# Performance work log

Hardware: AMD Instinct MI355X
Metric: run time of the kernel (lower is better)

## Reference

```python
import jax, jax.numpy as jnp
import numpy as np

IN_F = 2048
OUT_F = 2048
NNZ = 1048576
B = 8192


def setup_inputs() -> dict:
    key = jax.random.key(0)
    k1, k2, k3 = jax.random.split(key, 3)
    x = jax.random.normal(k1, (B, IN_F), dtype=jnp.float32)
    weights = (jax.random.normal(k2, (NNZ,), dtype=jnp.float32) * 0.02).astype(jnp.float16)
    coords = jax.random.randint(k3, (NNZ,), 0, OUT_F * IN_F, dtype=jnp.int64)
    return {"x": x, "weights": weights, "coords": coords}


def reference(x, weights, coords):
    # COO SpMV: out[b, row] += w * x[b, col] for each (row, col, w) triple.
    # coords are flat indices into the [OUT_F, IN_F] weight matrix.
    rows = coords // IN_F
    cols = coords % IN_F
    # Scatter-accumulate sparse weights into a dense matrix (duplicates add,
    # matching the kernel's atomic accumulation), then one batched matmul
    # replaces the per-row kernel launches of the original.
    W = jnp.zeros((OUT_F, IN_F), dtype=jnp.float32)
    W = W.at[rows, cols].add(weights.astype(jnp.float32))
    out = jnp.einsum('bi,oi->bo', x, W)  # [B, OUT_F] fp32, like the CL buffer
    return out.astype(x.dtype)
```

## Files before the change

kernel.cpp:

```cpp
#include <hip/hip_runtime.h>
#include <hip/hip_fp16.h>

#define IN_F   2048
#define OUT_F  2048
#define NNZ_   1048576
#define BATCH  8192
#define W_ROW0 6144
#define W_BASE ((size_t)W_ROW0 * OUT_F)

typedef __bf16 bf16x8 __attribute__((ext_vector_type(8)));
typedef float  f32x4  __attribute__((ext_vector_type(4)));

__device__ __forceinline__ float bfval(unsigned short b) {
    union { unsigned int u; float f; } t; t.u = ((unsigned int)b) << 16; return t.f;
}
__device__ __forceinline__ unsigned short f2bf(float f) {
    union { float f; unsigned int u; } v; v.f = f;
    unsigned int u = v.u; u += 0x7FFF + ((u >> 16) & 1);
    return (unsigned short)(u >> 16);
}
__device__ __forceinline__ float h2f(unsigned short b) {
    union { unsigned short u; __half h; } t; t.u = b; return __half2float(t.h);
}
__device__ __forceinline__ void gload_lds16(const void* g, void* l) {
    __builtin_amdgcn_global_load_lds(
        (const __attribute__((address_space(1))) unsigned int*)g,
        (__attribute__((address_space(3))) unsigned int*)l,
        16, 0, 0);
}

__global__ void prep_kernel(const float4* __restrict__ x,
                            ushort4* __restrict__ xb,
                            float4* __restrict__ Wz) {
    const int stride = gridDim.x * blockDim.x;
    const int t0 = blockIdx.x * blockDim.x + threadIdx.x;
    for (int i = t0; i < OUT_F * IN_F / 4; i += stride)
        Wz[i] = float4{0.f, 0.f, 0.f, 0.f};
    for (int i = t0; i < BATCH * IN_F / 4; i += stride) {
        float4 v = x[i];
        ushort4 o;
        o.x = f2bf(v.x); o.y = f2bf(v.y); o.z = f2bf(v.z); o.w = f2bf(v.w);
        xb[i] = o;
    }
}

__global__ void scatter_w_kernel(const unsigned short* __restrict__ wbits,
                                 const int* __restrict__ coords,
                                 float* __restrict__ W, int nnz) {
    __shared__ unsigned int sbf, sfh;
    if (threadIdx.x == 0) { sbf = 0u; sfh = 0u; }
    __syncthreads();
    unsigned int mbf = 0u, mfh = 0u;
    for (int i = threadIdx.x; i < 512; i += blockDim.x) {
        unsigned short b = wbits[i];
        unsigned int abf = (((unsigned int)b) << 16) & 0x7FFFFFFFu;
        unsigned int afh = (unsigned int)(b & 0x7FFF);
        mbf = mbf > abf ? mbf : abf;
        mfh = mfh > afh ? mfh : afh;
    }
    atomicMax(&sbf, mbf); atomicMax(&sfh, mfh);
    __syncthreads();
    union { unsigned int u; float f; } tb; tb.u = sbf;
    float bmax = tb.f;
    float hmax = h2f((unsigned short)sfh);
    int mode = (bmax > 1e-3f && bmax < 16.f) ? 0
             : (hmax > 1e-3f && hmax < 16.f) ? 1 : 2;

    int i = blockIdx.x * blockDim.x + threadIdx.x;
    if (i < nnz) {
        float v;
        if (mode == 0)      v = bfval(wbits[i]);
        else if (mode == 1) v = h2f(wbits[i]);
        else                v = ((const float*)wbits)[i];
        atomicAdd(&W[coords[i] & (OUT_F * IN_F - 1)], v);
    }
}

__global__ void f32_to_bf16_kernel(const float4* __restrict__ in,
                                   ushort4* __restrict__ out, int n4) {
    int s = gridDim.x * blockDim.x;
    for (int i = blockIdx.x * blockDim.x + threadIdx.x; i < n4; i += s) {
        float4 v = in[i];
        ushort4 o;
        o.x = f2bf(v.x); o.y = f2bf(v.y); o.z = f2bf(v.z); o.w = f2bf(v.w);
        out[i] = o;
    }
}

__global__ __launch_bounds__(512, 1) void gemm256_kernel(
    const unsigned short* __restrict__ xb,
    const unsigned short* __restrict__ wb,
    float* __restrict__ out) {
    constexpr int K = IN_F;
    constexpr int NT = K / 64;

    __shared__ __align__(16) unsigned short As[2][256 * 64];
    __shared__ __align__(16) unsigned short Bs[2][256 * 64];

    const int tid  = threadIdx.x;
    const int lane = tid & 63;
    const int wave = tid >> 6;
    const int wr   = wave >> 2;
    const int wc   = wave & 3;
    const int frow = lane & 15;
    const int klan = lane >> 4;
    const int s0   = klan ^ (lane & 7);

    const int flat = blockIdx.x;
    const int swz  = (flat & 7) * 32 + (flat >> 3);
    const int tm   = swz & 31;
    const int tn   = swz >> 5;

    const unsigned short* srcA = xb + (size_t)tm * 256 * K;
    const unsigned short* srcB = wb + (size_t)tn * 256 * K;

    const int rloc  = lane >> 3;
    const int sslot = (lane & 7) ^ rloc;

    f32x4 acc[8][4] = {};

    auto stage = [&](int buf, int kt) {
        const size_t coff = (size_t)kt * 64 + sslot * 8;
#pragma unroll
        for (int i = 0; i < 4; ++i) {
            const int row = i * 64 + wave * 8;
            gload_lds16(srcA + (size_t)(row + rloc) * K + coff,
                        &As[buf][row * 64]);
        }
#pragma unroll
        for (int i = 0; i < 4; ++i) {
            const int row = i * 64 + wave * 8;
            gload_lds16(srcB + (size_t)(row + rloc) * K + coff,
                        &Bs[buf][row * 64]);
        }
    };

    auto compute = [&](int buf) {
#pragma unroll
        for (int ks = 0; ks < 2; ++ks) {
            const int sl = s0 ^ (ks * 4);
            bf16x8 af[8], bg[4];
#pragma unroll
            for (int mf = 0; mf < 8; ++mf)
                af[mf] = *(const bf16x8*)
                    &As[buf][(wr * 128 + mf * 16 + frow) * 64 + sl * 8];
#pragma unroll
            for (int nf = 0; nf < 4; ++nf)
                bg[nf] = *(const bf16x8*)
                    &Bs[buf][(wc * 64 + nf * 16 + frow) * 64 + sl * 8];
            __builtin_amdgcn_s_setprio(1);
#pragma unroll
            for (int mf = 0; mf < 8; ++mf)
#pragma unroll
                for (int nf = 0; nf < 4; ++nf)
                    acc[mf][nf] = __builtin_amdgcn_mfma_f32_16x16x32_bf16(
                        af[mf], bg[nf], acc[mf][nf], 0, 0, 0);
            __builtin_amdgcn_s_setprio(0);
        }
    };

    stage(0, 0);
    stage(1, 1);

    for (int kt = 0; kt < NT - 2; ++kt) {
        asm volatile("s_waitcnt vmcnt(8)" ::: "memory");
        __builtin_amdgcn_s_barrier();
        compute(kt & 1);
        asm volatile("" ::: "memory");
        __builtin_amdgcn_s_barrier();
        stage(kt & 1, kt + 2);
    }
    asm volatile("s_waitcnt vmcnt(8)" ::: "memory");
    __builtin_amdgcn_s_barrier();
    compute((NT - 2) & 1);
    asm volatile("" ::: "memory");
    __builtin_amdgcn_s_barrier();
    asm volatile("s_waitcnt vmcnt(0)" ::: "memory");
    __builtin_amdgcn_s_barrier();
    compute((NT - 1) & 1);

    const int orow0 = tm * 256 + wr * 128 + klan * 4;
    const int ocol0 = tn * 256 + wc * 64 + frow;
#pragma unroll
    for (int mf = 0; mf < 8; ++mf)
#pragma unroll
        for (int nf = 0; nf < 4; ++nf)
#pragma unroll
            for (int r = 0; r < 4; ++r)
                out[(size_t)(orow0 + mf * 16 + r) * OUT_F + ocol0 + nf * 16]
                    = acc[mf][nf][r];
}

extern "C" void kernel_launch(void* const* d_in, const int* in_sizes, int n_in,
                              void* d_out, int out_size, void* d_ws, size_t ws_size,
                              hipStream_t stream) {
    const float*          x      = (const float*)d_in[0];
    const unsigned short* wbits  = (const unsigned short*)d_in[1];
    const int*            coords = (const int*)d_in[2];
    float*                out    = (float*)d_out;

    const size_t MB = 1024 * 1024;
    float*          W  = out + W_BASE;
    unsigned short* wb = (unsigned short*)d_ws;
    unsigned short* xb = (unsigned short*)((char*)d_ws + 8 * MB);
    (void)ws_size; (void)in_sizes; (void)n_in; (void)out_size;

    prep_kernel<<<2048, 256, 0, stream>>>((const float4*)x, (ushort4*)xb,
                                          (float4*)W);
    scatter_w_kernel<<<NNZ_ / 256, 256, 0, stream>>>(wbits, coords, W, NNZ_);
    f32_to_bf16_kernel<<<1024, 256, 0, stream>>>(
        (const float4*)W, (ushort4*)wb, OUT_F * IN_F / 4);

    gemm256_kernel<<<256, 512, 0, stream>>>(xb, wb, out);
}
```

Measured before the change: 165.4 us.

## Split GEMM k-step into phased LDS reads and MFMA groups with early prefetch

The per-k-tile compute is broken into four phases of 16 MFMAs, each preceded by a small batch of LDS fragment reads and separated by workgroup barriers. The next tile's global-to-LDS stage is issued before the last MFMA group instead of after the whole compute, which overlaps the load with math. The extra barriers and explicit lgkmcnt waits force lockstep between waves and may cost more in stalls than the overlap gains. Reusing the B fragments across the two M halves keeps register pressure bounded.

```diff
diff --git a/kernel.cpp b/kernel.cpp
--- a/kernel.cpp
+++ b/kernel.cpp
@@ -135,49 +135,63 @@
         }
     };
 
-    auto compute = [&](int buf) {
-#pragma unroll
-        for (int ks = 0; ks < 2; ++ks) {
-            const int sl = s0 ^ (ks * 4);
-            bf16x8 af[8], bg[4];
-#pragma unroll
-            for (int mf = 0; mf < 8; ++mf)
-                af[mf] = *(const bf16x8*)
-                    &As[buf][(wr * 128 + mf * 16 + frow) * 64 + sl * 8];
-#pragma unroll
-            for (int nf = 0; nf < 4; ++nf)
-                bg[nf] = *(const bf16x8*)
-                    &Bs[buf][(wc * 64 + nf * 16 + frow) * 64 + sl * 8];
-            __builtin_amdgcn_s_setprio(1);
-#pragma unroll
-            for (int mf = 0; mf < 8; ++mf)
-#pragma unroll
-                for (int nf = 0; nf < 4; ++nf)
-                    acc[mf][nf] = __builtin_amdgcn_mfma_f32_16x16x32_bf16(
-                        af[mf], bg[nf], acc[mf][nf], 0, 0, 0);
-            __builtin_amdgcn_s_setprio(0);
-        }
+    auto readA4 = [&](int buf, int mf0, int ks, bf16x8 (&af)[4]) {
+        const int sl = s0 ^ (ks * 4);
+#pragma unroll
+        for (int i = 0; i < 4; ++i)
+            af[i] = *(const bf16x8*)
+                &As[buf][(wr * 128 + (mf0 + i) * 16 + frow) * 64 + sl * 8];
+    };
+    auto readB4 = [&](int buf, int ks, bf16x8 (&bg)[4]) {
+        const int sl = s0 ^ (ks * 4);
+#pragma unroll
+        for (int i = 0; i < 4; ++i)
+            bg[i] = *(const bf16x8*)
+                &Bs[buf][(wc * 64 + i * 16 + frow) * 64 + sl * 8];
+    };
+    auto mfma16 = [&](int mf0, bf16x8 (&af)[4], bf16x8 (&bg)[4]) {
+        __builtin_amdgcn_s_setprio(1);
+#pragma unroll
+        for (int i = 0; i < 4; ++i)
+#pragma unroll
+            for (int j = 0; j < 4; ++j)
+                acc[mf0 + i][j] = __builtin_amdgcn_mfma_f32_16x16x32_bf16(
+                    af[i], bg[j], acc[mf0 + i][j], 0, 0, 0);
+        __builtin_amdgcn_s_setprio(0);
     };
 
     stage(0, 0);
     stage(1, 1);
 
-    for (int kt = 0; kt < NT - 2; ++kt) {
-        asm volatile("s_waitcnt vmcnt(8)" ::: "memory");
-        __builtin_amdgcn_s_barrier();
-        compute(kt & 1);
-        asm volatile("" ::: "memory");
-        __builtin_amdgcn_s_barrier();
-        stage(kt & 1, kt + 2);
-    }
-    asm volatile("s_waitcnt vmcnt(8)" ::: "memory");
-    __builtin_amdgcn_s_barrier();
-    compute((NT - 2) & 1);
-    asm volatile("" ::: "memory");
-    __builtin_amdgcn_s_barrier();
-    asm volatile("s_waitcnt vmcnt(0)" ::: "memory");
-    __builtin_amdgcn_s_barrier();
-    compute((NT - 1) & 1);
+    bf16x8 aL0[4], aL1[4], aH0[4], aH1[4], b0[4], b1[4];
+
+    for (int kt = 0; kt < NT; ++kt) {
+        const int buf = kt & 1;
+        if (kt < NT - 1) asm volatile("s_waitcnt vmcnt(8)" ::: "memory");
+        else             asm volatile("s_waitcnt vmcnt(0)" ::: "memory");
+        __builtin_amdgcn_s_barrier();
+
+        readA4(buf, 0, 0, aL0); readB4(buf, 0, b0);
+        __builtin_amdgcn_s_barrier();
+        asm volatile("s_waitcnt lgkmcnt(0)" ::: "memory");
+        mfma16(0, aL0, b0);
+        __builtin_amdgcn_s_barrier();
+
+        readA4(buf, 0, 1, aL1); readB4(buf, 1, b1);
+        __builtin_amdgcn_s_barrier();
+        asm volatile("s_waitcnt lgkmcnt(0)" ::: "memory");
+        mfma16(0, aL1, b1);
+        __builtin_amdgcn_s_barrier();
+
+        readA4(buf, 4, 0, aH0); readA4(buf, 4, 1, aH1);
+        __builtin_amdgcn_s_barrier();
+        asm volatile("s_waitcnt lgkmcnt(0)" ::: "memory");
+        mfma16(4, aH0, b0);
+        __builtin_amdgcn_s_barrier();
+
+        if (kt + 2 < NT) stage(buf, kt + 2);
+        mfma16(4, aH1, b1);
+    }
 
     const int orow0 = tm * 256 + wr * 128 + klan * 4;
     const int ocol0 = tn * 256 + wc * 64 + frow;
```

Result: slower. 169.7 us (+2.6%).
